# Kernel tuning notes

Hardware: AMD Instinct MI355X
Metric: run time of the kernel (lower is better)

The kernel has to match this reference:

```python
import jax, jax.numpy as jnp
import numpy as np

D_MODEL = 768
N_HEADS = 12
D_HEAD = D_MODEL // N_HEADS
B, L = 2, 4096


def setup_inputs() -> dict:
    key = jax.random.key(0)
    k1, k2, k3 = jax.random.split(key, 3)
    scale = 1.0 / np.sqrt(D_MODEL)
    return {
        "x": jax.random.normal(k1, (B, L, D_MODEL), dtype=jnp.float32),
        "w_qkv": jax.random.normal(k2, (D_MODEL, 3 * D_MODEL), dtype=jnp.float32) * scale,
        "b_qkv": jnp.zeros((3 * D_MODEL,), dtype=jnp.float32),
        "w_out": jax.random.normal(k3, (D_MODEL, D_MODEL), dtype=jnp.float32) * scale,
        "b_out": jnp.zeros((D_MODEL,), dtype=jnp.float32),
    }


def reference(x, w_qkv, b_qkv, w_out, b_out):
    b, l, d = x.shape
    # qkv projection -> (B, L, 3, H, Dh) -> split
    qkv = (x @ w_qkv + b_qkv).reshape(b, l, 3, N_HEADS, D_HEAD)
    qkv = jnp.transpose(qkv, (2, 0, 3, 1, 4))  # (3, B, H, L, Dh)
    q, k, v = qkv[0], qkv[1], qkv[2]
    # scaled scores with causal mask (dropout=0 / eval mode)
    att = jnp.einsum("bhqd,bhkd->bhqk", q, k) * (D_HEAD ** -0.5)
    causal = jnp.tril(jnp.ones((l, l), dtype=bool))
    att = jnp.where(causal, att, -jnp.inf)
    att = jax.nn.softmax(att, axis=-1)
    out = jnp.einsum("bhqk,bhkd->bhqd", att, v)  # (B, H, L, Dh)
    out = jnp.transpose(out, (0, 2, 1, 3)).reshape(b, l, d)
    return out @ w_out + b_out
```

## Files before the change

### kernel.cpp

```cpp
#include <hip/hip_runtime.h>
#include <hip/hip_bf16.h>

#define D_MODEL 768
#define NH 12
#define DHd 64
#define NB 2
#define SL 4096
#define BLr (NB*SL)
#define N3 (3*D_MODEL)
#define QSCALE 0.18033688011112042f

typedef __bf16 bf16x8 __attribute__((ext_vector_type(8)));
typedef float f32x4 __attribute__((ext_vector_type(4)));
typedef float f32x16 __attribute__((ext_vector_type(16)));
typedef unsigned int u32x4 __attribute__((ext_vector_type(4)));

__device__ __forceinline__ unsigned short f2bf(float f) {
  unsigned int u = __float_as_uint(f);
  u = (u + 0x7FFFu + ((u >> 16) & 1u)) >> 16;
  return (unsigned short)u;
}
__device__ __forceinline__ unsigned short bfc(float f) {
  __bf16 h = (__bf16)f;
  return __builtin_bit_cast(unsigned short, h);
}
__device__ __forceinline__ float fexp2(float x) {
  float r; asm("v_exp_f32 %0, %1" : "=v"(r) : "v"(x)); return r;
}
__device__ __forceinline__ unsigned int pk2(float lo, float hi2) {
  return ((unsigned int)bfc(hi2) << 16) | (unsigned int)bfc(lo);
}
__device__ __forceinline__ float vmax16(const f32x16& v) {
  float a = fmaxf(fmaxf(fmaxf(v[0],v[1]),fmaxf(v[2],v[3])),
                  fmaxf(fmaxf(v[4],v[5]),fmaxf(v[6],v[7])));
  float b = fmaxf(fmaxf(fmaxf(v[8],v[9]),fmaxf(v[10],v[11])),
                  fmaxf(fmaxf(v[12],v[13]),fmaxf(v[14],v[15])));
  return fmaxf(a,b);
}
__device__ __forceinline__ float vsum16(const f32x16& v) {
  float a = (v[0]+v[1])+(v[2]+v[3]);
  float b = (v[4]+v[5])+(v[6]+v[7]);
  float c = (v[8]+v[9])+(v[10]+v[11]);
  float d = (v[12]+v[13])+(v[14]+v[15]);
  return (a+b)+(c+d);
}

__global__ __launch_bounds__(256) void cast_f32_bf16(const float* __restrict__ in,
                                                     unsigned short* __restrict__ out, int n4) {
  int i = blockIdx.x * 256 + threadIdx.x;
  if (i >= n4) return;
  float4 v = reinterpret_cast<const float4*>(in)[i];
  ushort4 o;
  o.x = f2bf(v.x); o.y = f2bf(v.y); o.z = f2bf(v.z); o.w = f2bf(v.w);
  reinterpret_cast<ushort4*>(out)[i] = o;
}

__global__ __launch_bounds__(256) void transpose_cast(const float* __restrict__ in,
                                                      unsigned short* __restrict__ out,
                                                      int R, int C) {
  __shared__ float t[32][33];
  int c0 = blockIdx.x * 32, r0 = blockIdx.y * 32;
  int tx = threadIdx.x & 31, ty = threadIdx.x >> 5;
  #pragma unroll
  for (int i = 0; i < 32; i += 8) t[ty + i][tx] = in[(size_t)(r0 + ty + i) * C + c0 + tx];
  __syncthreads();
  #pragma unroll
  for (int i = 0; i < 32; i += 8) out[(size_t)(c0 + ty + i) * R + r0 + tx] = f2bf(t[tx][ty + i]);
}

template<int MODE>
__global__ __launch_bounds__(256) void gemm_bf16(const unsigned short* __restrict__ A,
                                                 const unsigned short* __restrict__ Bt,
                                                 const float* __restrict__ bias,
                                                 void* __restrict__ o0, void* __restrict__ o1,
                                                 void* __restrict__ o2,
                                                 int M, int N, int Kdim) {
  constexpr int LDT = 40;
  __shared__ unsigned short As[128 * LDT];
  __shared__ unsigned short Bs[128 * LDT];
  const int tid = threadIdx.x;
  const int lane = tid & 63, wave = tid >> 6;
  const int tm = blockIdx.x * 128, tn = blockIdx.y * 128;
  const int wm = (wave >> 1) * 64, wn = (wave & 1) * 64;
  const int fr = lane & 15, fk8 = (lane >> 4) * 8;
  const int srow = tid >> 2, scol = (tid & 3) * 8;

  f32x4 acc[4][4] = {};

  const unsigned short* Arow0 = A + (size_t)(tm + srow) * Kdim + scol;
  const unsigned short* Arow1 = A + (size_t)(tm + 64 + srow) * Kdim + scol;
  const unsigned short* Brow0 = Bt + (size_t)(tn + srow) * Kdim + scol;
  const unsigned short* Brow1 = Bt + (size_t)(tn + 64 + srow) * Kdim + scol;

  for (int k0 = 0; k0 < Kdim; k0 += 32) {
    ulonglong2 a0 = *(const ulonglong2*)(Arow0 + k0);
    ulonglong2 a1 = *(const ulonglong2*)(Arow1 + k0);
    ulonglong2 b0 = *(const ulonglong2*)(Brow0 + k0);
    ulonglong2 b1 = *(const ulonglong2*)(Brow1 + k0);
    __syncthreads();
    *(ulonglong2*)(As + srow * LDT + scol) = a0;
    *(ulonglong2*)(As + (64 + srow) * LDT + scol) = a1;
    *(ulonglong2*)(Bs + srow * LDT + scol) = b0;
    *(ulonglong2*)(Bs + (64 + srow) * LDT + scol) = b1;
    __syncthreads();

    bf16x8 af[4], bfr[4];
    #pragma unroll
    for (int i = 0; i < 4; i++) {
      af[i]  = *(const bf16x8*)(As + (wm + i * 16 + fr) * LDT + fk8);
      bfr[i] = *(const bf16x8*)(Bs + (wn + i * 16 + fr) * LDT + fk8);
    }
    #pragma unroll
    for (int i = 0; i < 4; i++)
      #pragma unroll
      for (int j = 0; j < 4; j++)
        acc[i][j] = __builtin_amdgcn_mfma_f32_16x16x32_bf16(af[i], bfr[j], acc[i][j], 0, 0, 0);
  }

  const int fq = (lane >> 4) * 4;
  if constexpr (MODE == 0) {
    unsigned short* Qb  = (unsigned short*)o0;
    unsigned short* Kb  = (unsigned short*)o1;
    unsigned short* Vtb = (unsigned short*)o2;
    #pragma unroll
    for (int j = 0; j < 4; j++) {
      int col = tn + wn + j * 16 + fr;
      float bv = bias[col];
      int which = col / D_MODEL;
      int hd = col % D_MODEL;
      int h = hd >> 6, d = hd & 63;
      #pragma unroll
      for (int i = 0; i < 4; i++) {
        #pragma unroll
        for (int r = 0; r < 4; r++) {
          int row = tm + wm + i * 16 + fq + r;
          int b = row >> 12, l = row & 4095;
          float v = acc[i][j][r] + bv;
          size_t hb = (size_t)b * NH + h;
          if (which == 0)      Qb[(hb * SL + l) * DHd + d] = bfc(v * QSCALE);
          else if (which == 1) Kb[(hb * SL + l) * DHd + d] = bfc(v);
          else                 Vtb[(hb * DHd + d) * SL + l] = bfc(v);
        }
      }
    }
  } else {
    float* Out = (float*)o0;
    #pragma unroll
    for (int i = 0; i < 4; i++)
      #pragma unroll
      for (int j = 0; j < 4; j++) {
        int col = tn + wn + j * 16 + fr;
        float bv = bias[col];
        #pragma unroll
        for (int r = 0; r < 4; r++) {
          int row = tm + wm + i * 16 + fq + r;
          Out[(size_t)row * N + col] = acc[i][j][r] + bv;
        }
      }
  }
}

#define PVSTEP(P, B, KS) do {                                              \
    unsigned int u0 = pk2(P[(B)+0], P[(B)+1]);                             \
    unsigned int u1 = pk2(P[(B)+2], P[(B)+3]);                             \
    unsigned int u2 = pk2(P[(B)+4], P[(B)+5]);                             \
    unsigned int u3 = pk2(P[(B)+6], P[(B)+7]);                             \
    unsigned int e0 = __shfl_xor(hi ? u0 : u2, 32);                        \
    unsigned int e1 = __shfl_xor(hi ? u1 : u3, 32);                        \
    u32x4 w;                                                               \
    w[0] = hi ? e0 : u0; w[1] = hi ? e1 : u1;                              \
    w[2] = hi ? u2 : e0; w[3] = hi ? u3 : e1;                              \
    bf16x8 pa = __builtin_bit_cast(bf16x8, w);                             \
    int bc = (32*(KS) + 16*hi) ^ vsw;                                      \
    bf16x8 vb0 = *(const bf16x8*)(vsb + l31*128 + bc);                     \
    oacc0 = __builtin_amdgcn_mfma_f32_32x32x16_bf16(pa, vb0, oacc0, 0,0,0);\
    bf16x8 vb1 = *(const bf16x8*)(vsb + (32+l31)*128 + bc);                \
    oacc1 = __builtin_amdgcn_mfma_f32_32x32x16_bf16(pa, vb1, oacc1, 0,0,0);\
  } while(0)

__global__ __launch_bounds__(256, 3) void attn_fwd(const unsigned short* __restrict__ Q,
                                                   const unsigned short* __restrict__ K,
                                                   const unsigned short* __restrict__ V,
                                                   unsigned short* __restrict__ O) {
  const int swzb = (blockIdx.x & 7) * 96 + (blockIdx.x >> 3);
  const int bh = swzb >> 5;
  const int qi = swzb & 31;
  const int tid = threadIdx.x;
  const int wave = tid >> 6, lane = tid & 63;
  const int g = wave >> 1, sub = wave & 1;
  const int l31 = lane & 31, hi = lane >> 5;
  const int tq = g ? (63 - qi) : qi;
  const int q0w = tq * 64 + sub * 32;
  const int nstage = 64 - qi;

  const unsigned short* Qbh = Q + (size_t)bh * SL * DHd;
  const unsigned short* Kbh = K + (size_t)bh * SL * DHd;
  const unsigned short* Vbh = V + (size_t)bh * DHd * SL;

  __shared__ unsigned short Ks[64 * 64];
  __shared__ unsigned short Vs[64 * 64];

  const char* qp = (const char*)Qbh + (size_t)(q0w + l31) * 128 + 16 * hi;
  bf16x8 qf0 = *(const bf16x8*)(qp);
  bf16x8 qf1 = *(const bf16x8*)(qp + 32);
  bf16x8 qf2 = *(const bf16x8*)(qp + 64);
  bf16x8 qf3 = *(const bf16x8*)(qp + 96);

  f32x16 oacc0 = {}, oacc1 = {};
  float m_i = -1e30f, l_i = 0.f;

  char* ksb = (char*)Ks;
  char* vsb = (char*)Vs;
  const int srow = tid >> 2;
  const int scB = (tid & 3) * 32;
  const int ssw = (srow & 7) << 4;
  const int vsw = (l31 & 7) << 4;

  const char* kgp = (const char*)Kbh + (size_t)srow * 128 + scB;
  const char* vgp = (const char*)Vbh + (size_t)srow * (SL * 2) + scB;

  ulonglong2 kr0 = *(const ulonglong2*)(kgp);
  ulonglong2 kr1 = *(const ulonglong2*)(kgp + 16);
  ulonglong2 vr0 = *(const ulonglong2*)(vgp);
  ulonglong2 vr1 = *(const ulonglong2*)(vgp + 16);

  for (int c = 0; c < nstage; c++) {
    __syncthreads();
    *(ulonglong2*)(ksb + srow * 128 + (scB ^ ssw)) = kr0;
    *(ulonglong2*)(ksb + srow * 128 + ((scB + 16) ^ ssw)) = kr1;
    *(ulonglong2*)(vsb + srow * 128 + (scB ^ ssw)) = vr0;
    *(ulonglong2*)(vsb + srow * 128 + ((scB + 16) ^ ssw)) = vr1;
    __syncthreads();
    if (c + 1 < nstage) {
      kr0 = *(const ulonglong2*)(kgp + (size_t)(c + 1) * 8192);
      kr1 = *(const ulonglong2*)(kgp + (size_t)(c + 1) * 8192 + 16);
      vr0 = *(const ulonglong2*)(vgp + (size_t)(c + 1) * 128);
      vr1 = *(const ulonglong2*)(vgp + (size_t)(c + 1) * 128 + 16);
    }

    if (c <= tq) {
      const int k0 = c * 64;
      const bool g1act = (k0 + 32 <= q0w);
      f32x16 s0 = {}, s1 = {};

      __builtin_amdgcn_s_setprio(1);
      {
        const char* kr = ksb + l31 * 128;
        bf16x8 a0 = *(const bf16x8*)(kr + ((16 * hi) ^ vsw));
        s0 = __builtin_amdgcn_mfma_f32_32x32x16_bf16(a0, qf0, s0, 0, 0, 0);
        bf16x8 a1 = *(const bf16x8*)(kr + ((32 + 16 * hi) ^ vsw));
        s0 = __builtin_amdgcn_mfma_f32_32x32x16_bf16(a1, qf1, s0, 0, 0, 0);
        bf16x8 a2 = *(const bf16x8*)(kr + ((64 + 16 * hi) ^ vsw));
        s0 = __builtin_amdgcn_mfma_f32_32x32x16_bf16(a2, qf2, s0, 0, 0, 0);
        bf16x8 a3 = *(const bf16x8*)(kr + ((96 + 16 * hi) ^ vsw));
        s0 = __builtin_amdgcn_mfma_f32_32x32x16_bf16(a3, qf3, s0, 0, 0, 0);
      }
      if (g1act) {
        const char* kr = ksb + (32 + l31) * 128;
        bf16x8 a0 = *(const bf16x8*)(kr + ((16 * hi) ^ vsw));
        s1 = __builtin_amdgcn_mfma_f32_32x32x16_bf16(a0, qf0, s1, 0, 0, 0);
        bf16x8 a1 = *(const bf16x8*)(kr + ((32 + 16 * hi) ^ vsw));
        s1 = __builtin_amdgcn_mfma_f32_32x32x16_bf16(a1, qf1, s1, 0, 0, 0);
        bf16x8 a2 = *(const bf16x8*)(kr + ((64 + 16 * hi) ^ vsw));
        s1 = __builtin_amdgcn_mfma_f32_32x32x16_bf16(a2, qf2, s1, 0, 0, 0);
        bf16x8 a3 = *(const bf16x8*)(kr + ((96 + 16 * hi) ^ vsw));
        s1 = __builtin_amdgcn_mfma_f32_32x32x16_bf16(a3, qf3, s1, 0, 0, 0);
      }
      __builtin_amdgcn_s_setprio(0);

      if (k0 == q0w) {
        #pragma unroll
        for (int r = 0; r < 16; r++) {
          int kvo = (r & 3) + 8 * (r >> 2) + 4 * hi;
          if (kvo > l31) s0[r] = -1e30f;
        }
      }
      if (g1act && (k0 + 32 == q0w)) {
        #pragma unroll
        for (int r = 0; r < 16; r++) {
          int kvo = (r & 3) + 8 * (r >> 2) + 4 * hi;
          if (kvo > l31) s1[r] = -1e30f;
        }
      }

      float pm = vmax16(s0);
      if (g1act) pm = fmaxf(pm, vmax16(s1));
      pm = fmaxf(pm, __shfl_xor(pm, 32));
      if (__any(pm > m_i + 10.f)) {
        float nm = fmaxf(m_i, pm);
        float sc = fexp2(m_i - nm);
        m_i = nm; l_i *= sc;
        #pragma unroll
        for (int r = 0; r < 16; r++) {
          float scr = __shfl(sc, (r & 3) + 8 * (r >> 2) + 4 * hi);
          oacc0[r] *= scr; oacc1[r] *= scr;
        }
      }
      #pragma unroll
      for (int r = 0; r < 16; r++) s0[r] = fexp2(s0[r] - m_i);
      float ts = vsum16(s0);
      if (g1act) {
        #pragma unroll
        for (int r = 0; r < 16; r++) s1[r] = fexp2(s1[r] - m_i);
        ts += vsum16(s1);
      }
      ts += __shfl_xor(ts, 32);
      l_i += ts;

      __builtin_amdgcn_s_setprio(1);
      PVSTEP(s0, 0, 0);
      PVSTEP(s0, 8, 1);
      if (g1act) {
        PVSTEP(s1, 0, 2);
        PVSTEP(s1, 8, 3);
      }
      __builtin_amdgcn_s_setprio(0);
    }
  }

  const int b = bh / NH, h = bh % NH;
  #pragma unroll
  for (int r = 0; r < 16; r++) {
    int qo = (r & 3) + 8 * (r >> 2) + 4 * hi;
    float lq = __shfl(l_i, qo);
    float inv = 1.0f / lq;
    size_t base = ((size_t)b * SL + q0w + qo) * D_MODEL + h * DHd;
    O[base + l31]      = bfc(oacc0[r] * inv);
    O[base + 32 + l31] = bfc(oacc1[r] * inv);
  }
}

extern "C" void kernel_launch(void* const* d_in, const int* in_sizes, int n_in,
                              void* d_out, int out_size, void* d_ws, size_t ws_size,
                              hipStream_t stream) {
  (void)in_sizes; (void)n_in; (void)out_size; (void)ws_size;
  const float* x     = (const float*)d_in[0];
  const float* w_qkv = (const float*)d_in[1];
  const float* b_qkv = (const float*)d_in[2];
  const float* w_out = (const float*)d_in[3];
  const float* b_out = (const float*)d_in[4];
  float* out = (float*)d_out;

  unsigned short* p = (unsigned short*)d_ws;
  unsigned short* xb    = p; p += (size_t)BLr * D_MODEL;
  unsigned short* wqkvT = p; p += (size_t)N3 * D_MODEL;
  unsigned short* woutT = p; p += (size_t)D_MODEL * D_MODEL;
  unsigned short* Qb    = p; p += (size_t)NB * NH * SL * DHd;
  unsigned short* Kb    = p; p += (size_t)NB * NH * SL * DHd;
  unsigned short* Vtb   = p; p += (size_t)NB * NH * SL * DHd;
  unsigned short* Ob    = p;

  cast_f32_bf16<<<(BLr * D_MODEL / 4 + 255) / 256, 256, 0, stream>>>(x, xb, BLr * D_MODEL / 4);
  transpose_cast<<<dim3(N3 / 32, D_MODEL / 32), 256, 0, stream>>>(w_qkv, wqkvT, D_MODEL, N3);
  transpose_cast<<<dim3(D_MODEL / 32, D_MODEL / 32), 256, 0, stream>>>(w_out, woutT, D_MODEL, D_MODEL);
  gemm_bf16<0><<<dim3(BLr / 128, N3 / 128), 256, 0, stream>>>(xb, wqkvT, b_qkv, Qb, Kb, Vtb,
                                                              BLr, N3, D_MODEL);
  attn_fwd<<<768, 256, 0, stream>>>(Qb, Kb, Vtb, Ob);
  gemm_bf16<1><<<dim3(BLr / 128, D_MODEL / 128), 256, 0, stream>>>(Ob, woutT, b_out, out,
                                                                   nullptr, nullptr,
                                                                   BLr, D_MODEL, D_MODEL);
}
```

Before: 210.2 us.

## Store Q/K/V in MFMA fragment order and load attention operands straight from global

The QKV projection epilogue now writes Q, K and V in a pre-swizzled layout that matches the per-lane MFMA operand fragments. The attention kernel drops the LDS staging and block-level barriers and loads K and V fragments directly from global memory with coalesced 16-byte loads. K is double-buffered in registers across iterations and each wave walks only its own causal range. The cost is more registers, with launch bounds lowered from 3 to 2 blocks per SM. K/V tiles shared by waves are no longer reused through LDS and are fetched from L2 by each wave.

```diff
diff --git a/kernel.cpp b/kernel.cpp
--- a/kernel.cpp
+++ b/kernel.cpp
@@ -119,9 +119,9 @@
 
   const int fq = (lane >> 4) * 4;
   if constexpr (MODE == 0) {
-    unsigned short* Qb  = (unsigned short*)o0;
-    unsigned short* Kb  = (unsigned short*)o1;
-    unsigned short* Vtb = (unsigned short*)o2;
+    unsigned short* Qf = (unsigned short*)o0;
+    unsigned short* Kf = (unsigned short*)o1;
+    unsigned short* Vf = (unsigned short*)o2;
     #pragma unroll
     for (int j = 0; j < 4; j++) {
       int col = tn + wn + j * 16 + fr;
@@ -137,9 +137,16 @@
           int b = row >> 12, l = row & 4095;
           float v = acc[i][j][r] + bv;
           size_t hb = (size_t)b * NH + h;
-          if (which == 0)      Qb[(hb * SL + l) * DHd + d] = bfc(v * QSCALE);
-          else if (which == 1) Kb[(hb * SL + l) * DHd + d] = bfc(v);
-          else                 Vtb[(hb * DHd + d) * SL + l] = bfc(v);
+          if (which == 2) {
+            size_t off = ((hb * 64 + (l >> 6)) * 8 + ((l >> 4) & 3) * 2 + (d >> 5)) * 512
+                       + (size_t)((d & 31) + 32 * ((l >> 3) & 1)) * 8 + (l & 7);
+            Vf[off] = bfc(v);
+          } else {
+            size_t off = ((hb * 128 + (l >> 5)) * 4 + (d >> 4)) * 512
+                       + (size_t)((l & 31) + 32 * ((d >> 3) & 1)) * 8 + (d & 7);
+            if (which == 0) Qf[off] = bfc(v * QSCALE);
+            else            Kf[off] = bfc(v);
+          }
         }
       }
     }
@@ -160,7 +167,9 @@
   }
 }
 
-#define PVSTEP(P, B, KS) do {                                              \
+struct KFrags { bf16x8 a[2][4]; };
+
+#define PVSTEP(P, B, VB0, VB1) do {                                        \
     unsigned int u0 = pk2(P[(B)+0], P[(B)+1]);                             \
     unsigned int u1 = pk2(P[(B)+2], P[(B)+3]);                             \
     unsigned int u2 = pk2(P[(B)+4], P[(B)+5]);                             \
@@ -171,16 +180,13 @@
     w[0] = hi ? e0 : u0; w[1] = hi ? e1 : u1;                              \
     w[2] = hi ? u2 : e0; w[3] = hi ? u3 : e1;                              \
     bf16x8 pa = __builtin_bit_cast(bf16x8, w);                             \
-    int bc = (32*(KS) + 16*hi) ^ vsw;                                      \
-    bf16x8 vb0 = *(const bf16x8*)(vsb + l31*128 + bc);                     \
-    oacc0 = __builtin_amdgcn_mfma_f32_32x32x16_bf16(pa, vb0, oacc0, 0,0,0);\
-    bf16x8 vb1 = *(const bf16x8*)(vsb + (32+l31)*128 + bc);                \
-    oacc1 = __builtin_amdgcn_mfma_f32_32x32x16_bf16(pa, vb1, oacc1, 0,0,0);\
+    oacc0 = __builtin_amdgcn_mfma_f32_32x32x16_bf16(pa, VB0, oacc0, 0,0,0);\
+    oacc1 = __builtin_amdgcn_mfma_f32_32x32x16_bf16(pa, VB1, oacc1, 0,0,0);\
   } while(0)
 
-__global__ __launch_bounds__(256, 3) void attn_fwd(const unsigned short* __restrict__ Q,
-                                                   const unsigned short* __restrict__ K,
-                                                   const unsigned short* __restrict__ V,
+__global__ __launch_bounds__(256, 2) void attn_fwd(const unsigned short* __restrict__ Qf,
+                                                   const unsigned short* __restrict__ Kf,
+                                                   const unsigned short* __restrict__ Vf,
                                                    unsigned short* __restrict__ O) {
   const int swzb = (blockIdx.x & 7) * 96 + (blockIdx.x >> 3);
   const int bh = swzb >> 5;
@@ -191,132 +197,113 @@
   const int l31 = lane & 31, hi = lane >> 5;
   const int tq = g ? (63 - qi) : qi;
   const int q0w = tq * 64 + sub * 32;
-  const int nstage = 64 - qi;
-
-  const unsigned short* Qbh = Q + (size_t)bh * SL * DHd;
-  const unsigned short* Kbh = K + (size_t)bh * SL * DHd;
-  const unsigned short* Vbh = V + (size_t)bh * DHd * SL;
-
-  __shared__ unsigned short Ks[64 * 64];
-  __shared__ unsigned short Vs[64 * 64];
-
-  const char* qp = (const char*)Qbh + (size_t)(q0w + l31) * 128 + 16 * hi;
-  bf16x8 qf0 = *(const bf16x8*)(qp);
-  bf16x8 qf1 = *(const bf16x8*)(qp + 32);
-  bf16x8 qf2 = *(const bf16x8*)(qp + 64);
-  bf16x8 qf3 = *(const bf16x8*)(qp + 96);
+  const int qb = tq * 2 + sub;
+
+  const char* Qb_ = (const char*)Qf + (((size_t)bh * 128 + qb) * 4) * 1024 + lane * 16;
+  const char* Kbh = (const char*)Kf + ((size_t)bh * 512) * 1024 + lane * 16;
+  const char* Vbh = (const char*)Vf + ((size_t)bh * 512) * 1024 + lane * 16;
+
+  bf16x8 qf[4];
+  #pragma unroll
+  for (int f = 0; f < 4; f++) qf[f] = *(const bf16x8*)(Qb_ + f * 1024);
 
   f32x16 oacc0 = {}, oacc1 = {};
   float m_i = -1e30f, l_i = 0.f;
 
-  char* ksb = (char*)Ks;
-  char* vsb = (char*)Vs;
-  const int srow = tid >> 2;
-  const int scB = (tid & 3) * 32;
-  const int ssw = (srow & 7) << 4;
-  const int vsw = (l31 & 7) << 4;
-
-  const char* kgp = (const char*)Kbh + (size_t)srow * 128 + scB;
-  const char* vgp = (const char*)Vbh + (size_t)srow * (SL * 2) + scB;
-
-  ulonglong2 kr0 = *(const ulonglong2*)(kgp);
-  ulonglong2 kr1 = *(const ulonglong2*)(kgp + 16);
-  ulonglong2 vr0 = *(const ulonglong2*)(vgp);
-  ulonglong2 vr1 = *(const ulonglong2*)(vgp + 16);
-
-  for (int c = 0; c < nstage; c++) {
-    __syncthreads();
-    *(ulonglong2*)(ksb + srow * 128 + (scB ^ ssw)) = kr0;
-    *(ulonglong2*)(ksb + srow * 128 + ((scB + 16) ^ ssw)) = kr1;
-    *(ulonglong2*)(vsb + srow * 128 + (scB ^ ssw)) = vr0;
-    *(ulonglong2*)(vsb + srow * 128 + ((scB + 16) ^ ssw)) = vr1;
-    __syncthreads();
-    if (c + 1 < nstage) {
-      kr0 = *(const ulonglong2*)(kgp + (size_t)(c + 1) * 8192);
-      kr1 = *(const ulonglong2*)(kgp + (size_t)(c + 1) * 8192 + 16);
-      vr0 = *(const ulonglong2*)(vgp + (size_t)(c + 1) * 128);
-      vr1 = *(const ulonglong2*)(vgp + (size_t)(c + 1) * 128 + 16);
-    }
-
-    if (c <= tq) {
-      const int k0 = c * 64;
-      const bool g1act = (k0 + 32 <= q0w);
-      f32x16 s0 = {}, s1 = {};
-
-      __builtin_amdgcn_s_setprio(1);
-      {
-        const char* kr = ksb + l31 * 128;
-        bf16x8 a0 = *(const bf16x8*)(kr + ((16 * hi) ^ vsw));
-        s0 = __builtin_amdgcn_mfma_f32_32x32x16_bf16(a0, qf0, s0, 0, 0, 0);
-        bf16x8 a1 = *(const bf16x8*)(kr + ((32 + 16 * hi) ^ vsw));
-        s0 = __builtin_amdgcn_mfma_f32_32x32x16_bf16(a1, qf1, s0, 0, 0, 0);
-        bf16x8 a2 = *(const bf16x8*)(kr + ((64 + 16 * hi) ^ vsw));
-        s0 = __builtin_amdgcn_mfma_f32_32x32x16_bf16(a2, qf2, s0, 0, 0, 0);
-        bf16x8 a3 = *(const bf16x8*)(kr + ((96 + 16 * hi) ^ vsw));
-        s0 = __builtin_amdgcn_mfma_f32_32x32x16_bf16(a3, qf3, s0, 0, 0, 0);
-      }
-      if (g1act) {
-        const char* kr = ksb + (32 + l31) * 128;
-        bf16x8 a0 = *(const bf16x8*)(kr + ((16 * hi) ^ vsw));
-        s1 = __builtin_amdgcn_mfma_f32_32x32x16_bf16(a0, qf0, s1, 0, 0, 0);
-        bf16x8 a1 = *(const bf16x8*)(kr + ((32 + 16 * hi) ^ vsw));
-        s1 = __builtin_amdgcn_mfma_f32_32x32x16_bf16(a1, qf1, s1, 0, 0, 0);
-        bf16x8 a2 = *(const bf16x8*)(kr + ((64 + 16 * hi) ^ vsw));
-        s1 = __builtin_amdgcn_mfma_f32_32x32x16_bf16(a2, qf2, s1, 0, 0, 0);
-        bf16x8 a3 = *(const bf16x8*)(kr + ((96 + 16 * hi) ^ vsw));
-        s1 = __builtin_amdgcn_mfma_f32_32x32x16_bf16(a3, qf3, s1, 0, 0, 0);
-      }
-      __builtin_amdgcn_s_setprio(0);
-
-      if (k0 == q0w) {
+  auto loadK = [&](KFrags& k, int c) {
+    const char* p = Kbh + (size_t)c * 8192;
+    #pragma unroll
+    for (int g2 = 0; g2 < 2; g2++)
+      #pragma unroll
+      for (int f = 0; f < 4; f++)
+        k.a[g2][f] = *(const bf16x8*)(p + g2 * 4096 + f * 1024);
+  };
+
+  auto body = [&](const KFrags& kc, KFrags* kn, int c, bool last) {
+    bf16x8 vv[4][2];
+    const char* vp = Vbh + (size_t)c * 8192;
+    #pragma unroll
+    for (int ks = 0; ks < 4; ks++) {
+      vv[ks][0] = *(const bf16x8*)(vp + ks * 2048);
+      vv[ks][1] = *(const bf16x8*)(vp + ks * 2048 + 1024);
+    }
+    if (kn) loadK(*kn, c + 1);
+
+    const bool g1act = !last || (sub == 1);
+    f32x16 s0 = {}, s1 = {};
+
+    __builtin_amdgcn_s_setprio(1);
+    #pragma unroll
+    for (int f = 0; f < 4; f++)
+      s0 = __builtin_amdgcn_mfma_f32_32x32x16_bf16(kc.a[0][f], qf[f], s0, 0, 0, 0);
+    if (g1act) {
+      #pragma unroll
+      for (int f = 0; f < 4; f++)
+        s1 = __builtin_amdgcn_mfma_f32_32x32x16_bf16(kc.a[1][f], qf[f], s1, 0, 0, 0);
+    }
+    __builtin_amdgcn_s_setprio(0);
+
+    if (last) {
+      if (sub == 0) {
         #pragma unroll
         for (int r = 0; r < 16; r++) {
           int kvo = (r & 3) + 8 * (r >> 2) + 4 * hi;
           if (kvo > l31) s0[r] = -1e30f;
         }
-      }
-      if (g1act && (k0 + 32 == q0w)) {
+      } else {
         #pragma unroll
         for (int r = 0; r < 16; r++) {
           int kvo = (r & 3) + 8 * (r >> 2) + 4 * hi;
           if (kvo > l31) s1[r] = -1e30f;
         }
       }
-
-      float pm = vmax16(s0);
-      if (g1act) pm = fmaxf(pm, vmax16(s1));
-      pm = fmaxf(pm, __shfl_xor(pm, 32));
-      if (__any(pm > m_i + 10.f)) {
-        float nm = fmaxf(m_i, pm);
-        float sc = fexp2(m_i - nm);
-        m_i = nm; l_i *= sc;
-        #pragma unroll
-        for (int r = 0; r < 16; r++) {
-          float scr = __shfl(sc, (r & 3) + 8 * (r >> 2) + 4 * hi);
-          oacc0[r] *= scr; oacc1[r] *= scr;
-        }
+    }
+
+    float pm = vmax16(s0);
+    if (g1act) pm = fmaxf(pm, vmax16(s1));
+    pm = fmaxf(pm, __shfl_xor(pm, 32));
+    if (__any(pm > m_i + 10.f)) {
+      float nm = fmaxf(m_i, pm);
+      float sc = fexp2(m_i - nm);
+      m_i = nm; l_i *= sc;
+      #pragma unroll
+      for (int r = 0; r < 16; r++) {
+        float scr = __shfl(sc, (r & 3) + 8 * (r >> 2) + 4 * hi);
+        oacc0[r] *= scr; oacc1[r] *= scr;
       }
-      #pragma unroll
-      for (int r = 0; r < 16; r++) s0[r] = fexp2(s0[r] - m_i);
-      float ts = vsum16(s0);
-      if (g1act) {
-        #pragma unroll
-        for (int r = 0; r < 16; r++) s1[r] = fexp2(s1[r] - m_i);
-        ts += vsum16(s1);
-      }
-      ts += __shfl_xor(ts, 32);
-      l_i += ts;
-
-      __builtin_amdgcn_s_setprio(1);
-      PVSTEP(s0, 0, 0);
-      PVSTEP(s0, 8, 1);
-      if (g1act) {
-        PVSTEP(s1, 0, 2);
-        PVSTEP(s1, 8, 3);
-      }
-      __builtin_amdgcn_s_setprio(0);
-    }
+    }
+    #pragma unroll
+    for (int r = 0; r < 16; r++) s0[r] = fexp2(s0[r] - m_i);
+    float ts = vsum16(s0);
+    if (g1act) {
+      #pragma unroll
+      for (int r = 0; r < 16; r++) s1[r] = fexp2(s1[r] - m_i);
+      ts += vsum16(s1);
+    }
+    ts += __shfl_xor(ts, 32);
+    l_i += ts;
+
+    __builtin_amdgcn_s_setprio(1);
+    PVSTEP(s0, 0, vv[0][0], vv[0][1]);
+    PVSTEP(s0, 8, vv[1][0], vv[1][1]);
+    if (g1act) {
+      PVSTEP(s1, 0, vv[2][0], vv[2][1]);
+      PVSTEP(s1, 8, vv[3][0], vv[3][1]);
+    }
+    __builtin_amdgcn_s_setprio(0);
+  };
+
+  KFrags kA, kB;
+  loadK(kA, 0);
+  int c = 0;
+  bool lastA = true;
+  while (c < tq) {
+    body(kA, &kB, c, false); c++;
+    if (c == tq) { lastA = false; break; }
+    body(kB, &kA, c, false); c++;
   }
+  if (lastA) body(kA, nullptr, tq, true);
+  else       body(kB, nullptr, tq, true);
 
   const int b = bh / NH, h = bh % NH;
   #pragma unroll
@@ -345,17 +332,17 @@
   unsigned short* xb    = p; p += (size_t)BLr * D_MODEL;
   unsigned short* wqkvT = p; p += (size_t)N3 * D_MODEL;
   unsigned short* woutT = p; p += (size_t)D_MODEL * D_MODEL;
-  unsigned short* Qb    = p; p += (size_t)NB * NH * SL * DHd;
-  unsigned short* Kb    = p; p += (size_t)NB * NH * SL * DHd;
-  unsigned short* Vtb   = p; p += (size_t)NB * NH * SL * DHd;
+  unsigned short* Qf    = p; p += (size_t)NB * NH * SL * DHd;
+  unsigned short* Kf    = p; p += (size_t)NB * NH * SL * DHd;
+  unsigned short* Vf    = p; p += (size_t)NB * NH * SL * DHd;
   unsigned short* Ob    = p;
 
   cast_f32_bf16<<<(BLr * D_MODEL / 4 + 255) / 256, 256, 0, stream>>>(x, xb, BLr * D_MODEL / 4);
   transpose_cast<<<dim3(N3 / 32, D_MODEL / 32), 256, 0, stream>>>(w_qkv, wqkvT, D_MODEL, N3);
   transpose_cast<<<dim3(D_MODEL / 32, D_MODEL / 32), 256, 0, stream>>>(w_out, woutT, D_MODEL, D_MODEL);
-  gemm_bf16<0><<<dim3(BLr / 128, N3 / 128), 256, 0, stream>>>(xb, wqkvT, b_qkv, Qb, Kb, Vtb,
+  gemm_bf16<0><<<dim3(BLr / 128, N3 / 128), 256, 0, stream>>>(xb, wqkvT, b_qkv, Qf, Kf, Vf,
                                                               BLr, N3, D_MODEL);
-  attn_fwd<<<768, 256, 0, stream>>>(Qb, Kb, Vtb, Ob);
+  attn_fwd<<<768, 256, 0, stream>>>(Qf, Kf, Vf, Ob);
   gemm_bf16<1><<<dim3(BLr / 128, D_MODEL / 128), 256, 0, stream>>>(Ob, woutT, b_out, out,
                                                                    nullptr, nullptr,
                                                                    BLr, D_MODEL, D_MODEL);
```

Result: slower. 218.6 us (+4.0%).
